# Kernel tuning notes

Measured on AMD Instinct MI355X. Metric: run time of the kernel, lower is better.

Reference implementation:

```python
import jax, jax.numpy as jnp
import numpy as np

B, L, C, N, D, FF, L2 = 1, 2400, 1536, 12, 128, 8960, 512
F_, H_, W_ = 2, 30, 40  # grid: L = F*H*W
EPS = 1e-6


def _rope_table(max_len=1024, d=D):
    # Wan rope_params: three bands of sizes d-4*(d//6), 2*(d//6), 2*(d//6)
    parts = [d - 4 * (d // 6), 2 * (d // 6), 2 * (d // 6)]
    pos = np.arange(max_len, dtype=np.float32)
    cs, ss = [], []
    for dp in parts:
        inv = 1.0 / (10000.0 ** (np.arange(0, dp, 2, dtype=np.float32) / dp))
        ang = np.outer(pos, inv)
        cs.append(np.cos(ang)); ss.append(np.sin(ang))
    return np.stack([np.concatenate(cs, 1), np.concatenate(ss, 1)], -1)  # [1024, d//2, 2]


def setup_inputs() -> dict:
    key = jax.random.key(0)
    ks = iter(jax.random.split(key, 48))
    def rn(shape, s=0.02):
        return jax.random.normal(next(ks), shape, dtype=jnp.float32) * s
    inp = dict(
        x=jax.random.normal(next(ks), (B, L, C), dtype=jnp.float32),
        e=rn((B, 1, 6, C), 0.5),
        context=jax.random.normal(next(ks), (B, L2, C), dtype=jnp.float32),
        freqs=jnp.asarray(_rope_table()),
        seq_lens=jnp.full((B,), L, dtype=jnp.int32),
        context_lens=jnp.full((B,), L2, dtype=jnp.int32),
        grid_sizes=jnp.array([[F_, H_, W_]], dtype=jnp.int32),
        modulation=rn((1, 6, C), 0.5),
    )
    for p in ('sa', 'ca'):
        for w in ('q', 'k', 'v', 'o'):
            inp[f'{p}_{w}_w'] = rn((C, C))
            inp[f'{p}_{w}_b'] = rn((C,))
        inp[f'{p}_nq_w'] = jnp.ones((C,), jnp.float32)
        inp[f'{p}_nk_w'] = jnp.ones((C,), jnp.float32)
    inp['ffn_w1'] = rn((C, FF)); inp['ffn_b1'] = rn((FF,))
    inp['ffn_w2'] = rn((FF, C)); inp['ffn_b2'] = rn((C,))
    return inp


def _rms_norm(x, w):
    v = jnp.mean(jnp.square(x), axis=-1, keepdims=True)
    return x * jax.lax.rsqrt(v + EPS) * w


def _layer_norm(x):
    m = jnp.mean(x, axis=-1, keepdims=True)
    v = jnp.mean(jnp.square(x - m), axis=-1, keepdims=True)
    return (x - m) * jax.lax.rsqrt(v + EPS)


def _apply_rope(x, freqs):
    # x: [B,S,N,D]; freqs: [1024, D//2, 2] (cos, sin). Wan default rope.
    c = D // 2
    p0, p1 = c - 2 * (c // 3), c // 3
    ft = jnp.broadcast_to(freqs[:F_, None, None, :p0], (F_, H_, W_, p0, 2))
    fh = jnp.broadcast_to(freqs[None, :H_, None, p0:p0 + p1], (F_, H_, W_, p1, 2))
    fw = jnp.broadcast_to(freqs[None, None, :W_, p0 + p1:], (F_, H_, W_, c - p0 - p1, 2))
    fr = jnp.concatenate([ft, fh, fw], axis=3).reshape(L, c, 2)
    cos = fr[..., 0][None, :, None, :]  # [1,S,1,c]
    sin = fr[..., 1][None, :, None, :]
    xp = x.reshape(B, x.shape[1], N, c, 2)  # interleaved (real, imag) pairs
    xr, xi = xp[..., 0], xp[..., 1]
    out = jnp.stack([xr * cos - xi * sin, xr * sin + xi * cos], axis=-1)
    return out.reshape(x.shape)


def _attention(q, k, v, k_len):
    # q:[B,Sq,N,D] k,v:[B,Sk,N,D]; dense softmax attention with k_lens mask
    scale = 1.0 / jnp.sqrt(jnp.float32(D))
    scores = jnp.einsum('bqnd,bknd->bnqk', q, k) * scale
    mask = jnp.arange(k.shape[1])[None, None, None, :] < k_len[:, None, None, None]
    scores = jnp.where(mask, scores, -jnp.inf)
    p = jax.nn.softmax(scores, axis=-1)
    return jnp.einsum('bnqk,bknd->bqnd', p, v)


def reference(x, e, context, freqs, seq_lens, context_lens, grid_sizes, modulation,
              sa_q_w, sa_q_b, sa_k_w, sa_k_b, sa_v_w, sa_v_b, sa_o_w, sa_o_b, sa_nq_w, sa_nk_w,
              ca_q_w, ca_q_b, ca_k_w, ca_k_b, ca_v_w, ca_v_b, ca_o_w, ca_o_b, ca_nq_w, ca_nk_w,
              ffn_w1, ffn_b1, ffn_w2, ffn_b2):
    # e: [B,1,6,C] (L1=1, broadcast over L == repeat_e); modulation: [1,6,C]
    em = modulation[None] + e  # [B,1,6,C]
    e0, e1, e2, e3, e4, e5 = (em[:, :, i] for i in range(6))  # each [B,1,C]
    # --- self attention with modulation ---
    h = e0 + _layer_norm(x) * (1.0 + e1)
    q = _rms_norm(h @ sa_q_w + sa_q_b, sa_nq_w).reshape(B, L, N, D)
    k = _rms_norm(h @ sa_k_w + sa_k_b, sa_nk_w).reshape(B, L, N, D)
    v = (h @ sa_v_w + sa_v_b).reshape(B, L, N, D)
    q = _apply_rope(q, freqs)
    k = _apply_rope(k, freqs)
    y = _attention(q, k, v, seq_lens).reshape(B, L, C)
    y = y @ sa_o_w + sa_o_b
    x = x + y * e2
    # --- cross attention (norm3 = Identity, cross_attn_norm=False) ---
    q = _rms_norm(x @ ca_q_w + ca_q_b, ca_nq_w).reshape(B, L, N, D)
    k = _rms_norm(context @ ca_k_w + ca_k_b, ca_nk_w).reshape(B, L2, N, D)
    v = (context @ ca_v_w + ca_v_b).reshape(B, L2, N, D)
    y = _attention(q, k, v, context_lens).reshape(B, L, C)
    x = x + (y @ ca_o_w + ca_o_b)
    # --- FFN with modulation ---
    h = e3 + _layer_norm(x) * (1.0 + e4)
    y = jax.nn.gelu(h @ ffn_w1 + ffn_b1, approximate=True) @ ffn_w2 + ffn_b2
    x = x + y * e5
    return x
```

## Files before the change

kernel.cpp:

```cpp
#include <hip/hip_runtime.h>
#include <cstddef>
#include <cstdint>

#define C_DIM   1536
#define L_SEQ   2400
#define L_CTX   512
#define N_HEADS 12
#define D_HEAD  128
#define FF_DIM  8960
#define F_GRID  2
#define H_GRID  30
#define W_GRID  40
#define EPS_F   1e-6f

#define ROPE_P0 22
#define ROPE_P1 43

typedef __attribute__((ext_vector_type(8))) short short8;
typedef __attribute__((ext_vector_type(4))) float f32x4;

__device__ inline unsigned short f2bf(float f) {
    union { float f; unsigned int u; } v; v.f = f;
    unsigned int r = v.u + 0x7FFF + ((v.u >> 16) & 1);
    return (unsigned short)(r >> 16);
}

#define GL2LDS(gp, lp) \
    __builtin_amdgcn_global_load_lds((const __attribute__((address_space(1))) void*)(gp), \
                                     (__attribute__((address_space(3))) void*)(lp), 16, 0, 0)


__global__ __launch_bounds__(256) void k_embed(const float* __restrict__ mod,
                                               const float* __restrict__ e,
                                               float* __restrict__ ev, int n) {
    int i = blockIdx.x * 256 + threadIdx.x;
    if (i < n) ev[i] = mod[i] + e[i];
}

__global__ __launch_bounds__(256) void k_catbias(float* __restrict__ dst,
                                                 const float* __restrict__ b0,
                                                 const float* __restrict__ b1,
                                                 const float* __restrict__ b2,
                                                 int ne, int n) {
    int i = blockIdx.x * 256 + threadIdx.x;
    if (i >= n) return;
    const float* s = (i < ne) ? b0 : (i < 2 * ne) ? b1 : b2;
    dst[i] = s[i % ne];
}

__global__ __launch_bounds__(256) void k_initbias(float* __restrict__ C,
                                                  const float* __restrict__ bias,
                                                  int n, int N) {
    int i4 = (blockIdx.x * 256 + threadIdx.x) * 4;
    if (i4 >= n) return;
    int col = i4 % N;
    *(float4*)(C + i4) = *(const float4*)(bias + col);
}

__global__ __launch_bounds__(256) void k_resid2(const float* __restrict__ a,
                                                const float* __restrict__ b,
                                                const float* __restrict__ ev, int ei,
                                                float* __restrict__ out,
                                                unsigned short* __restrict__ outb, int n) {
    int i = (blockIdx.x * 256 + threadIdx.x) * 2;
    if (i >= n) return;
    int c = i % C_DIM;
    float s0 = 1.f, s1 = 1.f;
    if (ei >= 0) {
        s0 = ev[ei * C_DIM + c];
        s1 = ev[ei * C_DIM + c + 1];
    }
    float2 av = *(const float2*)(a + i);
    float2 bv = *(const float2*)(b + i);
    float o0 = av.x + bv.x * s0;
    float o1 = av.y + bv.y * s1;
    *(float2*)(out + i) = make_float2(o0, o1);
    if (outb) {
        unsigned int pk = (unsigned int)f2bf(o0) | ((unsigned int)f2bf(o1) << 16);
        *(unsigned int*)(outb + i) = pk;
    }
}

__global__ __launch_bounds__(256) void k_tobf(const float* __restrict__ X,
                                              unsigned short* __restrict__ Y, int n) {
    int i = (blockIdx.x * 256 + threadIdx.x) * 2;
    if (i >= n) return;
    float2 v = *(const float2*)(X + i);
    unsigned int pk = (unsigned int)f2bf(v.x) | ((unsigned int)f2bf(v.y) << 16);
    *(unsigned int*)(Y + i) = pk;
}

__global__ __launch_bounds__(256) void k_lnmod_bf16(const float* __restrict__ X,
                                                    const float* __restrict__ ev,
                                                    int i0, int i1,
                                                    unsigned short* __restrict__ H) {
    __shared__ float rs[256];
    __shared__ float rs2[256];
    int row = blockIdx.x, tid = threadIdx.x;
    const float* xr = X + (size_t)row * C_DIM;
    float2 vals[3];
    float s = 0.f, s2 = 0.f;
#pragma unroll
    for (int i = 0; i < 3; ++i) {
        float2 v = *(const float2*)(xr + 2 * (tid + 256 * i));
        vals[i] = v;
        s += v.x + v.y; s2 += v.x * v.x + v.y * v.y;
    }
    rs[tid] = s; rs2[tid] = s2;
    __syncthreads();
    for (int st = 128; st > 0; st >>= 1) {
        if (tid < st) { rs[tid] += rs[tid + st]; rs2[tid] += rs2[tid + st]; }
        __syncthreads();
    }
    float mean = rs[0] * (1.0f / C_DIM);
    float var  = rs2[0] * (1.0f / C_DIM) - mean * mean;
    float rinv = rsqrtf(var + EPS_F);
    const float* E0 = ev + (size_t)i0 * C_DIM;
    const float* E1 = ev + (size_t)i1 * C_DIM;
    unsigned short* hr = H + (size_t)row * C_DIM;
#pragma unroll
    for (int i = 0; i < 3; ++i) {
        int c = 2 * (tid + 256 * i);
        float o0 = E0[c]     + (vals[i].x - mean) * rinv * (1.0f + E1[c]);
        float o1 = E0[c + 1] + (vals[i].y - mean) * rinv * (1.0f + E1[c + 1]);
        unsigned int pk = (unsigned int)f2bf(o0) | ((unsigned int)f2bf(o1) << 16);
        *(unsigned int*)(hr + c) = pk;
    }
}

__global__ __launch_bounds__(256) void k_rms_rope_bf16(const float* __restrict__ X,
                                                       const float* __restrict__ w,
                                                       const float* __restrict__ freqs,
                                                       int do_rope, float outscale,
                                                       unsigned short* __restrict__ Y,
                                                       int ldx) {
    __shared__ float rs[256];
    int row = blockIdx.x, tid = threadIdx.x;
    const float* xr = X + (size_t)row * ldx;
    float2 vals[3];
    float ss = 0.f;
#pragma unroll
    for (int i = 0; i < 3; ++i) {
        int p = tid + 256 * i;
        float2 v = *(const float2*)(xr + 2 * p);
        vals[i] = v;
        ss += v.x * v.x + v.y * v.y;
    }
    rs[tid] = ss;
    __syncthreads();
    for (int st = 128; st > 0; st >>= 1) {
        if (tid < st) rs[tid] += rs[tid + st];
        __syncthreads();
    }
    float rinv = rsqrtf(rs[0] * (1.0f / C_DIM) + EPS_F);
    int f = row / (H_GRID * W_GRID);
    int rem = row % (H_GRID * W_GRID);
    int hh = rem / W_GRID, ww = rem % W_GRID;
    unsigned short* yr = Y + (size_t)row * C_DIM;
#pragma unroll
    for (int i = 0; i < 3; ++i) {
        int p = tid + 256 * i;
        int c = 2 * p;
        float a = vals[i].x * rinv * w[c];
        float b = vals[i].y * rinv * w[c + 1];
        if (do_rope) {
            int j = p & 63;
            int idx = (j < ROPE_P0) ? f : (j < ROPE_P1) ? hh : ww;
            float cv = freqs[(idx * 64 + j) * 2 + 0];
            float sv = freqs[(idx * 64 + j) * 2 + 1];
            float na = a * cv - b * sv;
            float nb = a * sv + b * cv;
            a = na; b = nb;
        }
        a *= outscale; b *= outscale;
        unsigned int pk = (unsigned int)f2bf(a) | ((unsigned int)f2bf(b) << 16);
        *(unsigned int*)(yr + c) = pk;
    }
}

__global__ __launch_bounds__(256) void k_wt(const float* __restrict__ W,
                                            unsigned short* __restrict__ WT,
                                            int K, int N) {
    __shared__ float tile[32][33];
    int k0 = blockIdx.x * 32, n0 = blockIdx.y * 32;
    int t = threadIdx.x;
    int r = t >> 3, c4 = (t & 7) * 4;
    float4 v = *(const float4*)(W + (size_t)(k0 + r) * N + n0 + c4);
    tile[r][c4 + 0] = v.x; tile[r][c4 + 1] = v.y;
    tile[r][c4 + 2] = v.z; tile[r][c4 + 3] = v.w;
    __syncthreads();
    int n = t >> 3, k4 = (t & 7) * 4;
    uint2 o;
    o.x = (unsigned int)f2bf(tile[k4 + 0][n]) | ((unsigned int)f2bf(tile[k4 + 1][n]) << 16);
    o.y = (unsigned int)f2bf(tile[k4 + 2][n]) | ((unsigned int)f2bf(tile[k4 + 3][n]) << 16);
    *(uint2*)(WT + (size_t)(n0 + n) * K + k0 + k4) = o;
}

__global__ __launch_bounds__(256) void k_vt(const float* __restrict__ V,
                                            unsigned short* __restrict__ Vt, int Lk, int ldv) {
    __shared__ float tile[32][33];
    int k0 = blockIdx.x * 32, h = blockIdx.y, d0 = blockIdx.z * 32;
    int t = threadIdx.x;
    int k = t >> 3, d4 = (t & 7) * 4;
    float4 v = *(const float4*)(V + (size_t)(k0 + k) * ldv + h * D_HEAD + d0 + d4);
    tile[k][d4 + 0] = v.x; tile[k][d4 + 1] = v.y;
    tile[k][d4 + 2] = v.z; tile[k][d4 + 3] = v.w;
    __syncthreads();
    int d = t >> 3, k4 = (t & 7) * 4;
    uint2 o;
    o.x = (unsigned int)f2bf(tile[k4 + 0][d]) | ((unsigned int)f2bf(tile[k4 + 1][d]) << 16);
    o.y = (unsigned int)f2bf(tile[k4 + 2][d]) | ((unsigned int)f2bf(tile[k4 + 3][d]) << 16);
    *(uint2*)(Vt + (size_t)(h * D_HEAD + d0 + d) * Lk + k0 + k4) = o;
}

__global__ __launch_bounds__(256) void k_attn_mfma(const unsigned short* __restrict__ Qb,
                                                   const unsigned short* __restrict__ Kb,
                                                   const unsigned short* __restrict__ Vt,
                                                   unsigned short* __restrict__ O,
                                                   int Lq, int Lk) {
    __shared__ __align__(16) unsigned short Ks[32][136];
    __shared__ __align__(16) unsigned short Vs[128][40];
    __shared__ __align__(16) unsigned short Ps[4][16][40];
    const int tid = threadIdx.x;
    const int w = tid >> 6, lane = tid & 63;
    const int ln = lane & 15, lq = lane >> 4;
    const int h = blockIdx.y;
    const int q0 = blockIdx.x * 64 + w * 16;
    int qrow = q0 + ln; if (qrow >= Lq) qrow = Lq - 1;
    short8 qf[4];
#pragma unroll
    for (int c = 0; c < 4; ++c)
        qf[c] = *(const short8*)(Qb + (size_t)qrow * C_DIM + h * D_HEAD + c * 32 + lq * 8);
    f32x4 oacc[8];
#pragma unroll
    for (int t = 0; t < 8; ++t) oacc[t] = (f32x4){0.f, 0.f, 0.f, 0.f};
    float m_run[4] = {-3e38f, -3e38f, -3e38f, -3e38f};
    float l_run[4] = {0.f, 0.f, 0.f, 0.f};
    const float LOG2E = 1.4426950408889634f;

    for (int kb = 0; kb < Lk; kb += 32) {
        __syncthreads();
#pragma unroll
        for (int i = 0; i < 2; ++i) {
            int id = tid + i * 256;
            int r = id >> 4, c = id & 15;
            *(uint4*)&Ks[r][c * 8] =
                *(const uint4*)(Kb + (size_t)(kb + r) * C_DIM + h * D_HEAD + c * 8);
            int d = id >> 2, c2 = id & 3;
            *(uint4*)&Vs[d][c2 * 8] =
                *(const uint4*)(Vt + (size_t)(h * D_HEAD + d) * Lk + kb + c2 * 8);
        }
        __syncthreads();
        f32x4 c0 = (f32x4){0.f, 0.f, 0.f, 0.f};
        f32x4 c1 = (f32x4){0.f, 0.f, 0.f, 0.f};
#pragma unroll
        for (int c = 0; c < 4; ++c) {
            short8 b0 = *(const short8*)&Ks[ln][c * 32 + lq * 8];
            short8 b1 = *(const short8*)&Ks[16 + ln][c * 32 + lq * 8];
            c0 = __builtin_amdgcn_mfma_f32_16x16x32_bf16(qf[c], b0, c0, 0, 0, 0);
            c1 = __builtin_amdgcn_mfma_f32_16x16x32_bf16(qf[c], b1, c1, 0, 0, 0);
        }
        float alpha[4];
#pragma unroll
        for (int r = 0; r < 4; ++r) {
            float mx = fmaxf(c0[r], c1[r]);
            mx = fmaxf(mx, __shfl_xor(mx, 1));
            mx = fmaxf(mx, __shfl_xor(mx, 2));
            mx = fmaxf(mx, __shfl_xor(mx, 4));
            mx = fmaxf(mx, __shfl_xor(mx, 8));
            float mn = fmaxf(m_run[r], mx);
            alpha[r] = exp2f((m_run[r] - mn) * LOG2E);
            float p0 = exp2f((c0[r] - mn) * LOG2E);
            float p1 = exp2f((c1[r] - mn) * LOG2E);
            float s = p0 + p1;
            s += __shfl_xor(s, 1);
            s += __shfl_xor(s, 2);
            s += __shfl_xor(s, 4);
            s += __shfl_xor(s, 8);
            l_run[r] = l_run[r] * alpha[r] + s;
            m_run[r] = mn;
            Ps[w][lq * 4 + r][ln] = f2bf(p0);
            Ps[w][lq * 4 + r][16 + ln] = f2bf(p1);
        }
#pragma unroll
        for (int t = 0; t < 8; ++t)
#pragma unroll
            for (int r = 0; r < 4; ++r) oacc[t][r] *= alpha[r];
        short8 pa = *(const short8*)&Ps[w][ln][lq * 8];
#pragma unroll
        for (int t = 0; t < 8; ++t) {
            short8 bv = *(const short8*)&Vs[t * 16 + ln][lq * 8];
            oacc[t] = __builtin_amdgcn_mfma_f32_16x16x32_bf16(pa, bv, oacc[t], 0, 0, 0);
        }
    }
    float linv[4];
#pragma unroll
    for (int r = 0; r < 4; ++r) linv[r] = 1.0f / l_run[r];
#pragma unroll
    for (int t = 0; t < 8; ++t)
#pragma unroll
        for (int r = 0; r < 4; ++r) {
            int row = q0 + lq * 4 + r;
            if (row < Lq)
                O[(size_t)row * C_DIM + h * D_HEAD + t * 16 + ln] = f2bf(oacc[t][r] * linv[r]);
        }
}

__global__ __launch_bounds__(256) void k_gemm_bf16(const unsigned short* __restrict__ A,
                                                   const unsigned short* __restrict__ BT,
                                                   const float* __restrict__ bias,
                                                   float* __restrict__ Cf,
                                                   unsigned short* __restrict__ Cb,
                                                   int M, int N, int K, int Kc,
                                                   int gelu, int atomic) {
    __shared__ __align__(16) unsigned short As[128 * 32];
    __shared__ __align__(16) unsigned short Bs[128 * 32];
    const int tid = threadIdx.x;
    const int lane = tid & 63;
    const int w = tid >> 6;
    const int ln = lane & 15, lq = lane >> 4;
    const int wm = w >> 1, wn = w & 1;
    const int bm = blockIdx.y * 128, bn = blockIdx.x * 128;
    const int kb0 = blockIdx.z * Kc;

    int r0 = tid >> 2, c0 = (tid & 3) * 8;
    int ar0 = bm + r0;      if (ar0 >= M) ar0 = M - 1;
    int ar1 = bm + r0 + 64; if (ar1 >= M) ar1 = M - 1;
    const unsigned short* Ag0 = A + (size_t)ar0 * K + c0;
    const unsigned short* Ag1 = A + (size_t)ar1 * K + c0;
    const unsigned short* Bg0 = BT + (size_t)(bn + r0) * K + c0;
    const unsigned short* Bg1 = BT + (size_t)(bn + r0 + 64) * K + c0;
    unsigned short* Al0 = As + tid * 8;
    unsigned short* Al1 = As + 2048 + tid * 8;
    unsigned short* Bl0 = Bs + tid * 8;
    unsigned short* Bl1 = Bs + 2048 + tid * 8;

    f32x4 acc[4][4];
#pragma unroll
    for (int i = 0; i < 4; ++i)
#pragma unroll
        for (int j = 0; j < 4; ++j) acc[i][j] = (f32x4){0.f, 0.f, 0.f, 0.f};

    for (int kb = kb0; kb < kb0 + Kc; kb += 32) {
        __syncthreads();
        GL2LDS(Ag0 + kb, Al0);
        GL2LDS(Ag1 + kb, Al1);
        GL2LDS(Bg0 + kb, Bl0);
        GL2LDS(Bg1 + kb, Bl1);
        __syncthreads();
        short8 af[4], bf[4];
#pragma unroll
        for (int mi = 0; mi < 4; ++mi)
            af[mi] = *(const short8*)&As[(wm * 64 + mi * 16 + ln) * 32 + lq * 8];
#pragma unroll
        for (int ni = 0; ni < 4; ++ni)
            bf[ni] = *(const short8*)&Bs[(wn * 64 + ni * 16 + ln) * 32 + lq * 8];
#pragma unroll
        for (int mi = 0; mi < 4; ++mi)
#pragma unroll
            for (int ni = 0; ni < 4; ++ni)
                acc[mi][ni] = __builtin_amdgcn_mfma_f32_16x16x32_bf16(af[mi], bf[ni],
                                                                      acc[mi][ni], 0, 0, 0);
    }

#pragma unroll
    for (int ni = 0; ni < 4; ++ni) {
        int col = bn + wn * 64 + ni * 16 + ln;
        float bv = atomic ? 0.f : bias[col];
#pragma unroll
        for (int mi = 0; mi < 4; ++mi) {
#pragma unroll
            for (int r = 0; r < 4; ++r) {
                int row = bm + wm * 64 + mi * 16 + lq * 4 + r;
                if (row >= M) continue;
                if (atomic) {
                    atomicAdd(Cf + (size_t)row * N + col, acc[mi][ni][r]);
                } else if (gelu) {
                    float v = acc[mi][ni][r] + bv;
                    float u = 0.7978845608028654f * (v + 0.044715f * v * v * v);
                    float ex = __expf(2.f * u);
                    float t = 1.f - 2.f / (ex + 1.f);
                    Cb[(size_t)row * N + col] = f2bf(0.5f * v * (1.f + t));
                } else {
                    Cf[(size_t)row * N + col] = acc[mi][ni][r] + bv;
                }
            }
        }
    }
}

extern "C" void kernel_launch(void* const* d_in, const int* in_sizes, int n_in,
                              void* d_out, int out_size, void* d_ws, size_t ws_size,
                              hipStream_t stream) {
    const float* x          = (const float*)d_in[0];
    const float* e          = (const float*)d_in[1];
    const float* context    = (const float*)d_in[2];
    const float* freqs      = (const float*)d_in[3];
    const float* modulation = (const float*)d_in[7];
    const float* sa_q_w = (const float*)d_in[8];
    const float* sa_q_b = (const float*)d_in[9];
    const float* sa_k_w = (const float*)d_in[10];
    const float* sa_k_b = (const float*)d_in[11];
    const float* sa_v_w = (const float*)d_in[12];
    const float* sa_v_b = (const float*)d_in[13];
    const float* sa_o_w = (const float*)d_in[14];
    const float* sa_o_b = (const float*)d_in[15];
    const float* sa_nq  = (const float*)d_in[16];
    const float* sa_nk  = (const float*)d_in[17];
    const float* ca_q_w = (const float*)d_in[18];
    const float* ca_q_b = (const float*)d_in[19];
    const float* ca_k_w = (const float*)d_in[20];
    const float* ca_k_b = (const float*)d_in[21];
    const float* ca_v_w = (const float*)d_in[22];
    const float* ca_v_b = (const float*)d_in[23];
    const float* ca_o_w = (const float*)d_in[24];
    const float* ca_o_b = (const float*)d_in[25];
    const float* ca_nq  = (const float*)d_in[26];
    const float* ca_nk  = (const float*)d_in[27];
    const float* ffn_w1 = (const float*)d_in[28];
    const float* ffn_b1 = (const float*)d_in[29];
    const float* ffn_w2 = (const float*)d_in[30];
    const float* ffn_b2 = (const float*)d_in[31];

    const size_t LC = (size_t)L_SEQ * C_DIM;
    const size_t WMAX = (size_t)C_DIM * FF_DIM;
    char* p = (char*)d_ws;
    float* ev   = (float*)p;            p += 6 * C_DIM * sizeof(float);
    float* Bcat = (float*)p;            p += 3 * C_DIM * sizeof(float);
    float* Xcur = (float*)p;            p += LC * sizeof(float);
    float* Ebuf = (float*)p;            p += LC * sizeof(float);
    float* QKV  = (float*)p;            p += 3 * LC * sizeof(float);
    unsigned short* Ab = (unsigned short*)p;  p += LC * sizeof(short);
    unsigned short* Xb = (unsigned short*)p;  p += LC * sizeof(short);
    unsigned short* Qb = (unsigned short*)p;  p += LC * sizeof(short);
    unsigned short* Kb = (unsigned short*)p;  p += LC * sizeof(short);
    unsigned short* Vt = (unsigned short*)p;  p += LC * sizeof(short);
    unsigned short* Ob = (unsigned short*)p;  p += LC * sizeof(short);
    unsigned short* W0 = (unsigned short*)p;  p += WMAX * sizeof(short);
    unsigned short* W1 = (unsigned short*)p;  p += WMAX * sizeof(short);
    unsigned short* Fb = (unsigned short*)QKV;
    float* Pq    = QKV;
    float* ctxKV = QKV + LC;

    const int nLC = (int)LC;
    const float SCALE = 0.08838834764831845f;
    dim3 blk(256);
    dim3 g_qkv(4608 / 128, 19, 1);
    dim3 g_proj_s4(C_DIM / 128, 19, 4);
    dim3 g_ctxkv_s4(3072 / 128, L_CTX / 128, 4);
    dim3 g_ff1(FF_DIM / 128, 19, 1);
    dim3 g_attn((L_SEQ + 63) / 64, N_HEADS);
    dim3 g_vt_s(L_SEQ / 32, N_HEADS, 4);
    dim3 g_vt_c(L_CTX / 32, N_HEADS, 4);
    dim3 g_wt_cc(C_DIM / 32, C_DIM / 32);
    dim3 g_wt_w1(C_DIM / 32, FF_DIM / 32);
    dim3 g_wt_w2(FF_DIM / 32, C_DIM / 32);
    dim3 g_half(nLC / 512);
    dim3 g_init_cc(nLC / 1024);
    dim3 g_init_kv(L_CTX * 3072 / 1024);

    k_embed<<<dim3((6 * C_DIM + 255) / 256), blk, 0, stream>>>(modulation, e, ev, 6 * C_DIM);

    k_catbias<<<dim3((3 * C_DIM + 255) / 256), blk, 0, stream>>>(Bcat, sa_q_b, sa_k_b, sa_v_b,
                                                                 C_DIM, 3 * C_DIM);
    k_wt<<<g_wt_cc, blk, 0, stream>>>(sa_q_w, W0, C_DIM, C_DIM);
    k_wt<<<g_wt_cc, blk, 0, stream>>>(sa_k_w, W0 + (size_t)C_DIM * C_DIM, C_DIM, C_DIM);
    k_wt<<<g_wt_cc, blk, 0, stream>>>(sa_v_w, W0 + (size_t)2 * C_DIM * C_DIM, C_DIM, C_DIM);
    k_lnmod_bf16<<<dim3(L_SEQ), blk, 0, stream>>>(x, ev, 0, 1, Ab);
    k_gemm_bf16<<<g_qkv, blk, 0, stream>>>(Ab, W0, Bcat, QKV, nullptr,
                                           L_SEQ, 4608, C_DIM, C_DIM, 0, 0);
    k_wt<<<g_wt_cc, blk, 0, stream>>>(sa_o_w, W1, C_DIM, C_DIM);
    k_rms_rope_bf16<<<dim3(L_SEQ), blk, 0, stream>>>(QKV, sa_nq, freqs, 1, SCALE, Qb, 4608);
    k_rms_rope_bf16<<<dim3(L_SEQ), blk, 0, stream>>>(QKV + C_DIM, sa_nk, freqs, 1, 1.0f, Kb, 4608);
    k_vt<<<g_vt_s, blk, 0, stream>>>(QKV + 2 * C_DIM, Vt, L_SEQ, 4608);
    k_attn_mfma<<<g_attn, blk, 0, stream>>>(Qb, Kb, Vt, Ob, L_SEQ, L_SEQ);
    k_initbias<<<g_init_cc, blk, 0, stream>>>(Ebuf, sa_o_b, nLC, C_DIM);
    k_gemm_bf16<<<g_proj_s4, blk, 0, stream>>>(Ob, W1, nullptr, Ebuf, nullptr,
                                               L_SEQ, C_DIM, C_DIM, 384, 0, 1);
    k_resid2<<<g_half, blk, 0, stream>>>(x, Ebuf, ev, 2, Xcur, Xb, nLC);

    k_wt<<<g_wt_cc, blk, 0, stream>>>(ca_q_w, W0, C_DIM, C_DIM);
    k_wt<<<g_wt_cc, blk, 0, stream>>>(ca_k_w, W1, C_DIM, C_DIM);
    k_wt<<<g_wt_cc, blk, 0, stream>>>(ca_v_w, W1 + (size_t)C_DIM * C_DIM, C_DIM, C_DIM);
    k_tobf<<<dim3(L_CTX * C_DIM / 512), blk, 0, stream>>>(context, Ab, L_CTX * C_DIM);
    k_catbias<<<dim3((2 * C_DIM + 255) / 256), blk, 0, stream>>>(Bcat, ca_k_b, ca_v_b, nullptr,
                                                                 C_DIM, 2 * C_DIM);
    k_initbias<<<g_init_cc, blk, 0, stream>>>(Pq, ca_q_b, nLC, C_DIM);
    k_gemm_bf16<<<g_proj_s4, blk, 0, stream>>>(Xb, W0, nullptr, Pq, nullptr,
                                               L_SEQ, C_DIM, C_DIM, 384, 0, 1);
    k_initbias<<<g_init_kv, blk, 0, stream>>>(ctxKV, Bcat, L_CTX * 3072, 3072);
    k_gemm_bf16<<<g_ctxkv_s4, blk, 0, stream>>>(Ab, W1, nullptr, ctxKV, nullptr,
                                                L_CTX, 3072, C_DIM, 384, 0, 1);
    k_rms_rope_bf16<<<dim3(L_SEQ), blk, 0, stream>>>(Pq, ca_nq, freqs, 0, SCALE, Qb, C_DIM);
    k_rms_rope_bf16<<<dim3(L_CTX), blk, 0, stream>>>(ctxKV, ca_nk, freqs, 0, 1.0f, Kb, 3072);
    k_vt<<<g_vt_c, blk, 0, stream>>>(ctxKV + C_DIM, Vt, L_CTX, 3072);
    k_attn_mfma<<<g_attn, blk, 0, stream>>>(Qb, Kb, Vt, Ob, L_SEQ, L_CTX);
    k_wt<<<g_wt_cc, blk, 0, stream>>>(ca_o_w, W0, C_DIM, C_DIM);
    k_initbias<<<g_init_cc, blk, 0, stream>>>(Ebuf, ca_o_b, nLC, C_DIM);
    k_gemm_bf16<<<g_proj_s4, blk, 0, stream>>>(Ob, W0, nullptr, Ebuf, nullptr,
                                               L_SEQ, C_DIM, C_DIM, 384, 0, 1);
    k_resid2<<<g_half, blk, 0, stream>>>(Xcur, Ebuf, (const float*)nullptr, -1, Xcur, nullptr, nLC);

    k_wt<<<g_wt_w1, blk, 0, stream>>>(ffn_w1, W1, C_DIM, FF_DIM);
    k_lnmod_bf16<<<dim3(L_SEQ), blk, 0, stream>>>(Xcur, ev, 3, 4, Ab);
    k_gemm_bf16<<<g_ff1, blk, 0, stream>>>(Ab, W1, ffn_b1, nullptr, Fb,
                                           L_SEQ, FF_DIM, C_DIM, C_DIM, 1, 0);
    k_wt<<<g_wt_w2, blk, 0, stream>>>(ffn_w2, W0, FF_DIM, C_DIM);
    k_initbias<<<g_init_cc, blk, 0, stream>>>(Ebuf, ffn_b2, nLC, C_DIM);
    k_gemm_bf16<<<g_proj_s4, blk, 0, stream>>>(Fb, W0, nullptr, Ebuf, nullptr,
                                               L_SEQ, C_DIM, FF_DIM, 2240, 0, 1);
    k_resid2<<<g_half, blk, 0, stream>>>(Xcur, Ebuf, ev, 5, (float*)d_out, nullptr, nLC);
}
```

Before: 1.123 ms.

## Add 256x256 ping-pong pipelined bf16 GEMM kernel for FFN matmuls

Introduces a new 512-thread GEMM kernel with 256x256 output tiles, double-buffered LDS staging through direct global-to-LDS loads, explicit vmcnt waits, and interleaved MFMA phases with priority hints. Both FFN GEMMs (FF1 with fused GELU, and split-K FF2 with atomics) now use it instead of the 128x128 kernel. The larger tile raises operand reuse and the hand-scheduled pipeline aims to overlap loads with MFMA. The cost is more registers and LDS per block, fewer blocks (edge tiles padded on M up to 2560), and tricky manual wait counts that could be fragile.

```diff
diff --git a/kernel.cpp b/kernel.cpp
--- a/kernel.cpp
+++ b/kernel.cpp
@@ -28,6 +28,11 @@
 #define GL2LDS(gp, lp) \
     __builtin_amdgcn_global_load_lds((const __attribute__((address_space(1))) void*)(gp), \
                                      (__attribute__((address_space(3))) void*)(lp), 16, 0, 0)
+
+#define VMCNT6() asm volatile("s_waitcnt vmcnt(6)" ::: "memory")
+#define VMCNT0() asm volatile("s_waitcnt vmcnt(0)" ::: "memory")
+#define LGKM0()  asm volatile("s_waitcnt lgkmcnt(0)" ::: "memory")
+#define BAR()    __builtin_amdgcn_s_barrier()
 
 
 __global__ __launch_bounds__(256) void k_embed(const float* __restrict__ mod,
@@ -372,6 +377,160 @@
 #pragma unroll
             for (int r = 0; r < 4; ++r) {
                 int row = bm + wm * 64 + mi * 16 + lq * 4 + r;
+                if (row >= M) continue;
+                if (atomic) {
+                    atomicAdd(Cf + (size_t)row * N + col, acc[mi][ni][r]);
+                } else if (gelu) {
+                    float v = acc[mi][ni][r] + bv;
+                    float u = 0.7978845608028654f * (v + 0.044715f * v * v * v);
+                    float ex = __expf(2.f * u);
+                    float t = 1.f - 2.f / (ex + 1.f);
+                    Cb[(size_t)row * N + col] = f2bf(0.5f * v * (1.f + t));
+                } else {
+                    Cf[(size_t)row * N + col] = acc[mi][ni][r] + bv;
+                }
+            }
+        }
+    }
+}
+
+__global__ __launch_bounds__(512, 2) void k_gemm256(const unsigned short* __restrict__ A,
+                                                    const unsigned short* __restrict__ BT,
+                                                    const float* __restrict__ bias,
+                                                    float* __restrict__ Cf,
+                                                    unsigned short* __restrict__ Cb,
+                                                    int M, int N, int K, int Kc,
+                                                    int gelu, int atomic) {
+    __shared__ __align__(16) unsigned short lds[2][2][2][128 * 64];
+    const int tid = threadIdx.x;
+    const int wid = tid >> 6, lane = tid & 63;
+    const int ln = lane & 15, lq = lane >> 4;
+    const int wm = wid >> 2, wn = wid & 3;
+    const int bm = blockIdx.y * 256, bn = blockIdx.x * 256;
+    const int kb0 = blockIdx.z * Kc;
+    const int NT = Kc >> 6;
+    const int NI = (NT + 1) >> 1;
+
+    const int rr = tid >> 3, cc = (tid & 7) * 8;
+    const unsigned short* aP[4];
+    const unsigned short* bP[4];
+#pragma unroll
+    for (int g = 0; g < 4; ++g) {
+        int ar = bm + g * 64 + rr; if (ar >= M) ar = M - 1;
+        aP[g] = A + (size_t)ar * K + cc + kb0;
+        bP[g] = BT + (size_t)(bn + g * 64 + rr) * K + cc + kb0;
+    }
+
+    f32x4 acc[8][4];
+#pragma unroll
+    for (int i = 0; i < 8; ++i)
+#pragma unroll
+        for (int j = 0; j < 4; ++j) acc[i][j] = (f32x4){0.f, 0.f, 0.f, 0.f};
+
+    short8 af[4][2], bf0[2][2], bf1[2][2];
+
+    const unsigned short* A0 = &lds[0][0][wm][0];
+    const unsigned short* A1 = &lds[1][0][wm][0];
+    const unsigned short* B0 = &lds[0][1][wn >> 1][0];
+    const unsigned short* B1 = &lds[1][1][wn >> 1][0];
+
+    auto stgA = [&](unsigned short* dst, int h, int kt) {
+        GL2LDS(aP[h * 2 + 0] + (size_t)kt * 64, dst + tid * 8);
+        GL2LDS(aP[h * 2 + 1] + (size_t)kt * 64, dst + 4096 + tid * 8);
+    };
+    auto stgB = [&](unsigned short* dst, int h, int kt) {
+        GL2LDS(bP[h * 2 + 0] + (size_t)kt * 64, dst + tid * 8);
+        GL2LDS(bP[h * 2 + 1] + (size_t)kt * 64, dst + 4096 + tid * 8);
+    };
+    auto rdA = [&](const unsigned short* Ab_, int mh) {
+#pragma unroll
+        for (int m4 = 0; m4 < 4; ++m4)
+#pragma unroll
+            for (int ks = 0; ks < 2; ++ks)
+                af[m4][ks] = *(const short8*)&Ab_[(mh * 64 + m4 * 16 + ln) * 64 + ks * 32 + lq * 8];
+    };
+    auto rdB = [&](const unsigned short* Bb_, int nh, short8 (&bfX)[2][2]) {
+#pragma unroll
+        for (int n2 = 0; n2 < 2; ++n2)
+#pragma unroll
+            for (int ks = 0; ks < 2; ++ks)
+                bfX[n2][ks] = *(const short8*)&Bb_[((wn & 1) * 64 + (nh * 2 + n2) * 16 + ln) * 64 +
+                                                   ks * 32 + lq * 8];
+    };
+    auto mm = [&](int mh, int nh, short8 (&bfX)[2][2]) {
+        __builtin_amdgcn_s_setprio(1);
+#pragma unroll
+        for (int m4 = 0; m4 < 4; ++m4)
+#pragma unroll
+            for (int n2 = 0; n2 < 2; ++n2)
+#pragma unroll
+                for (int ks = 0; ks < 2; ++ks)
+                    acc[mh * 4 + m4][nh * 2 + n2] = __builtin_amdgcn_mfma_f32_16x16x32_bf16(
+                        af[m4][ks], bfX[n2][ks], acc[mh * 4 + m4][nh * 2 + n2], 0, 0, 0);
+        __builtin_amdgcn_s_setprio(0);
+    };
+
+    stgB(&lds[0][1][0][0], 0, 0); stgB(&lds[0][1][1][0], 1, 0);
+    stgA(&lds[0][0][0][0], 0, 0);
+    stgA(&lds[0][0][1][0], 1, 0);
+    stgB(&lds[1][1][0][0], 0, 1);
+    stgA(&lds[1][0][0][0], 0, 1); stgB(&lds[1][1][1][0], 1, 1);
+    VMCNT6(); BAR();
+
+    for (int k0 = 0; k0 < NI; ++k0) {
+        const int a = 2 * k0, bT = a + 1;
+        const bool last = (k0 == NI - 1);
+        const bool hasB = (bT < NT);
+        rdA(A0, 0); rdB(B0, 0, bf0);
+        if (hasB) stgA(&lds[1][0][1][0], 1, bT);
+        BAR(); LGKM0();
+        mm(0, 0, bf0);
+        BAR();
+        rdB(B0, 1, bf1);
+        BAR(); LGKM0();
+        mm(0, 1, bf1);
+        BAR();
+        rdA(A0, 1);
+        if (a + 2 < NT) { stgB(&lds[0][1][0][0], 0, a + 2); stgB(&lds[0][1][1][0], 1, a + 2); }
+        BAR(); LGKM0();
+        mm(1, 1, bf1);
+        BAR();
+        if (a + 2 < NT) stgA(&lds[0][0][0][0], 0, a + 2);
+        BAR();
+        mm(1, 0, bf0);
+        if (!hasB) { BAR(); break; }
+        if (last) { VMCNT0(); } else { VMCNT6(); }
+        BAR();
+        rdA(A1, 0); rdB(B1, 0, bf0);
+        if (a + 2 < NT) stgA(&lds[0][0][1][0], 1, a + 2);
+        BAR(); LGKM0();
+        mm(0, 0, bf0);
+        BAR();
+        rdB(B1, 1, bf1);
+        BAR(); LGKM0();
+        mm(0, 1, bf1);
+        BAR();
+        rdA(A1, 1);
+        if (bT + 2 < NT) stgB(&lds[1][1][0][0], 0, bT + 2);
+        BAR(); LGKM0();
+        mm(1, 1, bf1);
+        BAR();
+        if (bT + 2 < NT) { stgA(&lds[1][0][0][0], 0, bT + 2); stgB(&lds[1][1][1][0], 1, bT + 2); }
+        BAR();
+        mm(1, 0, bf0);
+        if (k0 >= NI - 2) { VMCNT0(); } else { VMCNT6(); }
+        BAR();
+    }
+
+#pragma unroll
+    for (int ni = 0; ni < 4; ++ni) {
+        int col = bn + wn * 64 + ni * 16 + ln;
+        float bv = atomic ? 0.f : bias[col];
+#pragma unroll
+        for (int mi = 0; mi < 8; ++mi) {
+#pragma unroll
+            for (int r = 0; r < 4; ++r) {
+                int row = bm + wm * 128 + mi * 16 + lq * 4 + r;
                 if (row >= M) continue;
                 if (atomic) {
                     atomicAdd(Cf + (size_t)row * N + col, acc[mi][ni][r]);
@@ -445,10 +604,12 @@
     const int nLC = (int)LC;
     const float SCALE = 0.08838834764831845f;
     dim3 blk(256);
+    dim3 blk512(512);
     dim3 g_qkv(4608 / 128, 19, 1);
     dim3 g_proj_s4(C_DIM / 128, 19, 4);
     dim3 g_ctxkv_s4(3072 / 128, L_CTX / 128, 4);
-    dim3 g_ff1(FF_DIM / 128, 19, 1);
+    dim3 g_ff1_256(FF_DIM / 256, 10, 1);
+    dim3 g_ff2_256(C_DIM / 256, 10, 4);
     dim3 g_attn((L_SEQ + 63) / 64, N_HEADS);
     dim3 g_vt_s(L_SEQ / 32, N_HEADS, 4);
     dim3 g_vt_c(L_CTX / 32, N_HEADS, 4);
@@ -503,11 +664,11 @@
 
     k_wt<<<g_wt_w1, blk, 0, stream>>>(ffn_w1, W1, C_DIM, FF_DIM);
     k_lnmod_bf16<<<dim3(L_SEQ), blk, 0, stream>>>(Xcur, ev, 3, 4, Ab);
-    k_gemm_bf16<<<g_ff1, blk, 0, stream>>>(Ab, W1, ffn_b1, nullptr, Fb,
-                                           L_SEQ, FF_DIM, C_DIM, C_DIM, 1, 0);
+    k_gemm256<<<g_ff1_256, blk512, 0, stream>>>(Ab, W1, ffn_b1, nullptr, Fb,
+                                                L_SEQ, FF_DIM, C_DIM, C_DIM, 1, 0);
     k_wt<<<g_wt_w2, blk, 0, stream>>>(ffn_w2, W0, FF_DIM, C_DIM);
     k_initbias<<<g_init_cc, blk, 0, stream>>>(Ebuf, ffn_b2, nLC, C_DIM);
-    k_gemm_bf16<<<g_proj_s4, blk, 0, stream>>>(Fb, W0, nullptr, Ebuf, nullptr,
-                                               L_SEQ, C_DIM, FF_DIM, 2240, 0, 1);
+    k_gemm256<<<g_ff2_256, blk512, 0, stream>>>(Fb, W0, nullptr, Ebuf, nullptr,
+                                                L_SEQ, C_DIM, FF_DIM, 2240, 0, 1);
     k_resid2<<<g_half, blk, 0, stream>>>(Xcur, Ebuf, ev, 5, (float*)d_out, nullptr, nLC);
 }
```

Result: slower. 1.156 ms (+2.9%).
